# Performance work log

Hardware: AMD Instinct MI355X
Metric: run time of the kernel (lower is better)

Reference implementation:

```python
import jax, jax.numpy as jnp
import numpy as np
from jax import lax

B, C, H, W = 4, 64, 64, 64
CH = C // 2  # edge_detect hidden channels
BN_EPS = 1e-5


def conv1x1(x, w, b):
    # x: (B,C,H,W), w: (O,C), b: (O,)
    return jnp.einsum('bchw,oc->bohw', x, w) + b[None, :, None, None]


def setup_inputs() -> dict:
    key = jax.random.key(0)
    ks = jax.random.split(key, 12)
    s = 1.0 / np.sqrt(C)
    inp = {
        'x': jax.random.normal(ks[0], (B, C, H, W), jnp.float32),
        'Wq': jax.random.normal(ks[1], (C, C), jnp.float32) * s,
        'bq': jnp.zeros((C,), jnp.float32),
        'Wk': jax.random.normal(ks[2], (C, C), jnp.float32) * s,
        'bk': jnp.zeros((C,), jnp.float32),
        'Wv': jax.random.normal(ks[3], (C, C), jnp.float32) * s,
        'bv': jnp.zeros((C,), jnp.float32),
        'We1': jax.random.normal(ks[4], (CH, C, 3, 3), jnp.float32) * (1.0 / np.sqrt(C * 9)),
        'be1': jnp.zeros((CH,), jnp.float32),
        'bn_w': jnp.ones((CH,), jnp.float32),
        'bn_b': jnp.zeros((CH,), jnp.float32),
        'bn_mean': jnp.zeros((CH,), jnp.float32),
        'bn_var': jnp.ones((CH,), jnp.float32),
        'We2': jax.random.normal(ks[5], (1, CH), jnp.float32) * (1.0 / np.sqrt(CH)),
        'be2': jnp.zeros((1,), jnp.float32),
        'gamma': jax.random.normal(ks[6], (1,), jnp.float32) * 0.1,
        'beta': jax.random.normal(ks[7], (1,), jnp.float32) * 0.1,
    }
    return inp


def reference(x, Wq, bq, Wk, bk, Wv, bv, We1, be1, bn_w, bn_b, bn_mean, bn_var, We2, be2, gamma, beta):
    b, c, h, w = x.shape
    hw = h * w
    q = conv1x1(x, Wq, bq).reshape(b, c, hw).transpose(0, 2, 1)  # (B,HW,C)
    k = conv1x1(x, Wk, bk).reshape(b, c, hw)                      # (B,C,HW)
    v = conv1x1(x, Wv, bv).reshape(b, c, hw)                      # (B,C,HW)

    energy = jnp.einsum('bnc,bcm->bnm', q, k)                      # (B,HW,HW)
    attention = jax.nn.softmax(energy, axis=-1)

    # edge_detect: 3x3 conv -> BN (eval stats) -> ReLU -> 1x1 conv -> sigmoid
    e = lax.conv_general_dilated(x, We1, (1, 1), 'SAME',
                                 dimension_numbers=('NCHW', 'OIHW', 'NCHW'))
    e = e + be1[None, :, None, None]
    e = (e - bn_mean[None, :, None, None]) * jax.lax.rsqrt(bn_var + BN_EPS)[None, :, None, None]
    e = e * bn_w[None, :, None, None] + bn_b[None, :, None, None]
    e = jax.nn.relu(e)
    e = conv1x1(e, We2, be2)                                       # (B,1,H,W)
    edge = jax.nn.sigmoid(e).reshape(b, 1, hw)                     # (B,1,HW)

    fa = attention * (1.0 + beta[0] * edge)                        # broadcast over query dim
    denom = jnp.maximum(jnp.sum(jnp.abs(fa), axis=2, keepdims=True), 1e-12)
    fa = fa / denom                                                # L1 renorm along keys

    out = jnp.einsum('bcm,bnm->bcn', v, fa).reshape(b, c, h, w)
    return gamma[0] * out + x
```

## Files before the change

kernel.cpp:

```cpp
#include <hip/hip_runtime.h>
#include <hip/hip_bf16.h>

typedef unsigned short u16;
typedef __attribute__((ext_vector_type(8))) __bf16 bf16x8;
typedef __attribute__((ext_vector_type(4))) float f32x4;


__device__ __forceinline__ u16 f2bf(float f) {
    unsigned u = __builtin_bit_cast(unsigned, f);
    u += 0x7FFFu + ((u >> 16) & 1u);
    return (u16)(u >> 16);
}
__device__ __forceinline__ float bf2f(u16 v) {
    unsigned u = ((unsigned)v) << 16;
    return __builtin_bit_cast(float, u);
}

__global__ __launch_bounds__(256) void qkv_edge_kernel(
    const float* __restrict__ x,
    const float* __restrict__ Wq, const float* __restrict__ bq,
    const float* __restrict__ Wk, const float* __restrict__ bk,
    const float* __restrict__ Wv, const float* __restrict__ bv,
    const float* __restrict__ We1, const float* __restrict__ be1,
    const float* __restrict__ bn_w, const float* __restrict__ bn_b,
    const float* __restrict__ bn_mean, const float* __restrict__ bn_var,
    const float* __restrict__ We2, const float* __restrict__ be2,
    const float* __restrict__ beta,
    u16* __restrict__ Qt, u16* __restrict__ Kt, u16* __restrict__ Vm,
    float* __restrict__ wkey)
{
    __shared__ __align__(16) u16 sm[33280];
    const int t = threadIdx.x;
    const int wv = t >> 6, lane = t & 63;
    const int quad = lane >> 4, l15 = lane & 15;

    if (blockIdx.x < 256) {
        u16* Wl   = sm;
        u16* xt_s = sm + 13824;
        u16* vt   = sm + 13824 + 4224;
        const int b = blockIdx.x >> 6;
        const int n0 = (blockIdx.x & 63) << 6;

        const float* Wmat[3] = {Wq, Wk, Wv};
#pragma unroll
        for (int m = 0; m < 3; ++m)
#pragma unroll
            for (int i = 0; i < 4; ++i) {
                int u = t + i * 256;
                float4 w4 = *reinterpret_cast<const float4*>(Wmat[m] + u * 4);
                int row = u >> 4, col = (u & 15) * 4;
                uint2 pk;
                pk.x = (unsigned)f2bf(w4.x) | ((unsigned)f2bf(w4.y) << 16);
                pk.y = (unsigned)f2bf(w4.z) | ((unsigned)f2bf(w4.w) << 16);
                *reinterpret_cast<uint2*>(&Wl[(m * 64 + row) * 72 + col]) = pk;
            }
        for (int i = 0; i < 16; ++i) {
            int lin = t + i * 256;
            int c = lin >> 6, nn = lin & 63;
            xt_s[nn * 66 + c] = f2bf(x[(size_t)(b * 64 + c) * 4096 + n0 + nn]);
        }
        __syncthreads();

        bf16x8 bx[2];
#pragma unroll
        for (int h = 0; h < 2; ++h)
            bx[h] = *reinterpret_cast<const bf16x8*>(
                &xt_s[(wv * 16 + l15) * 66 + h * 32 + quad * 8]);

        f32x4 d[3][4];
#pragma unroll
        for (int m = 0; m < 3; ++m)
#pragma unroll
            for (int mt = 0; mt < 4; ++mt) d[m][mt] = (f32x4){0.f, 0.f, 0.f, 0.f};

#pragma unroll
        for (int h = 0; h < 2; ++h)
#pragma unroll
            for (int m = 0; m < 3; ++m)
#pragma unroll
                for (int mt = 0; mt < 4; ++mt) {
                    bf16x8 af = *reinterpret_cast<const bf16x8*>(
                        &Wl[(m * 64 + mt * 16 + l15) * 72 + h * 32 + quad * 8]);
                    d[m][mt] = __builtin_amdgcn_mfma_f32_16x16x32_bf16(af, bx[h], d[m][mt], 0, 0, 0);
                }

        const float* bias[3] = {bq, bk, bv};
        const float L2E = 1.44269504f;
#pragma unroll
        for (int m = 0; m < 3; ++m)
#pragma unroll
            for (int mt = 0; mt < 4; ++mt) {
                float4 bi = *reinterpret_cast<const float4*>(bias[m] + mt * 16 + quad * 4);
                d[m][mt][0] += bi.x; d[m][mt][1] += bi.y; d[m][mt][2] += bi.z; d[m][mt][3] += bi.w;
                if (m == 0) {
                    d[m][mt][0] *= L2E; d[m][mt][1] *= L2E;
                    d[m][mt][2] *= L2E; d[m][mt][3] *= L2E;
                }
            }

        const int rowchunk = (n0 >> 4) + wv;
#pragma unroll
        for (int m = 0; m < 2; ++m) {
            u16* base = (m == 0 ? Qt : Kt) + (size_t)b * 262144;
#pragma unroll
            for (int mt = 0; mt < 4; ++mt) {
                uint2 pk;
                pk.x = (unsigned)f2bf(d[m][mt][0]) | ((unsigned)f2bf(d[m][mt][1]) << 16);
                pk.y = (unsigned)f2bf(d[m][mt][2]) | ((unsigned)f2bf(d[m][mt][3]) << 16);
                *reinterpret_cast<uint2*>(
                    base + ((size_t)(rowchunk * 8 + mt * 2 + (quad >> 1))) * 128 +
                    l15 * 8 + (quad & 1) * 4) = pk;
            }
        }
#pragma unroll
        for (int mt = 0; mt < 4; ++mt)
#pragma unroll
            for (int r = 0; r < 4; ++r)
                vt[(mt * 16 + quad * 4 + r) * 72 + wv * 16 + l15] = f2bf(d[2][mt][r]);
        __syncthreads();
        {
            u16* Vb_st = Vm + (size_t)b * 262144;
            const int kt = n0 >> 6;
#pragma unroll
            for (int i = 0; i < 2; ++i) {
                int unit = t + i * 256;
                int f = unit >> 7, hq = (unit >> 4) & 7, cl = unit & 15;
                const u16* src = &vt[(f * 16 + cl) * 72 + hq * 8];
                uint4 v4 = *reinterpret_cast<const uint4*>(src);
                *reinterpret_cast<uint4*>(
                    Vb_st + ((size_t)((kt * 4 + f) * 8 + hq)) * 128 + cl * 8) = v4;
            }
        }
    } else {
        u16* Ae_s = sm;
        u16* xr_s = sm + 18688;
        const int eb = blockIdx.x - 256;
        const int b = eb >> 6, h = eb & 63;

        if (t < 192) {
            int kh = t / 64, rem = t & 63;
            int col = (rem >> 5) * 65, ci2 = (rem & 31) * 2;
            *reinterpret_cast<unsigned*>(&xr_s[(kh * 66 + col) * 72 + ci2]) = 0u;
        }
#pragma unroll
        for (int i = 0; i < 18; ++i) {
            int u = t + i * 256;
            int ch = u / 144;
            int rem = u - ch * 144;
            int p = rem >> 4, cig = (rem & 15) * 4;
            const float* src = We1 + ch * 576 + cig * 9 + p;
            float a = src[0], b2 = src[9], c2 = src[18], d2 = src[27];
            uint2 pk;
            pk.x = (unsigned)f2bf(a) | ((unsigned)f2bf(b2) << 16);
            pk.y = (unsigned)f2bf(c2) | ((unsigned)f2bf(d2) << 16);
            *reinterpret_cast<uint2*>(&Ae_s[ch * 584 + p * 64 + cig]) = pk;
        }
#pragma unroll
        for (int i = 0; i < 12; ++i) {
            int u = t + i * 256;
            int w = u & 63, cig = (u >> 6) & 15, kh = u >> 10;
            int hs = h + kh - 1;
            float v0 = 0.f, v1 = 0.f, v2 = 0.f, v3 = 0.f;
            if ((unsigned)hs < 64u) {
                const float* src = x + ((size_t)(b * 64 + cig * 4) * 64 + hs) * 64 + w;
                v0 = src[0]; v1 = src[4096]; v2 = src[8192]; v3 = src[12288];
            }
            uint2 pk;
            pk.x = (unsigned)f2bf(v0) | ((unsigned)f2bf(v1) << 16);
            pk.y = (unsigned)f2bf(v2) | ((unsigned)f2bf(v3) << 16);
            *reinterpret_cast<uint2*>(&xr_s[(kh * 66 + w + 1) * 72 + cig * 4]) = pk;
        }
        __syncthreads();

        f32x4 e[2];
        e[0] = (f32x4){0.f, 0.f, 0.f, 0.f};
        e[1] = (f32x4){0.f, 0.f, 0.f, 0.f};
#pragma unroll
        for (int p = 0; p < 9; ++p) {
            const int kh = p / 3, kw = p - kh * 3;
#pragma unroll
            for (int half = 0; half < 2; ++half) {
                bf16x8 bfr = *reinterpret_cast<const bf16x8*>(
                    &xr_s[(kh * 66 + wv * 16 + l15 + kw) * 72 + half * 32 + quad * 8]);
#pragma unroll
                for (int mt = 0; mt < 2; ++mt) {
                    bf16x8 af = *reinterpret_cast<const bf16x8*>(
                        &Ae_s[(mt * 16 + l15) * 584 + p * 64 + half * 32 + quad * 8]);
                    e[mt] = __builtin_amdgcn_mfma_f32_16x16x32_bf16(af, bfr, e[mt], 0, 0, 0);
                }
            }
        }
        float partial = 0.f;
#pragma unroll
        for (int mt = 0; mt < 2; ++mt) {
            float4 bw = *reinterpret_cast<const float4*>(bn_w    + mt * 16 + quad * 4);
            float4 bb = *reinterpret_cast<const float4*>(bn_b    + mt * 16 + quad * 4);
            float4 bm = *reinterpret_cast<const float4*>(bn_mean + mt * 16 + quad * 4);
            float4 bv2 = *reinterpret_cast<const float4*>(bn_var + mt * 16 + quad * 4);
            float4 b1 = *reinterpret_cast<const float4*>(be1     + mt * 16 + quad * 4);
            float4 w2 = *reinterpret_cast<const float4*>(We2     + mt * 16 + quad * 4);
            float sc, sh;
            sc = bw.x * rsqrtf(bv2.x + 1e-5f); sh = (b1.x - bm.x) * sc + bb.x;
            partial += fmaxf(e[mt][0] * sc + sh, 0.f) * w2.x;
            sc = bw.y * rsqrtf(bv2.y + 1e-5f); sh = (b1.y - bm.y) * sc + bb.y;
            partial += fmaxf(e[mt][1] * sc + sh, 0.f) * w2.y;
            sc = bw.z * rsqrtf(bv2.z + 1e-5f); sh = (b1.z - bm.z) * sc + bb.z;
            partial += fmaxf(e[mt][2] * sc + sh, 0.f) * w2.z;
            sc = bw.w * rsqrtf(bv2.w + 1e-5f); sh = (b1.w - bm.w) * sc + bb.w;
            partial += fmaxf(e[mt][3] * sc + sh, 0.f) * w2.w;
        }
        partial += __shfl_xor(partial, 16);
        partial += __shfl_xor(partial, 32);
        if (lane < 16) {
            float s = partial + be2[0];
            float sg = 1.f / (1.f + __expf(-s));
            wkey[(size_t)b * 4096 + h * 64 + wv * 16 + lane] = 1.f + beta[0] * sg;
        }
    }
}

template <int NSPLIT>
__global__ __launch_bounds__(128, 4) void attn_kernel(
    const u16* __restrict__ Qt, const u16* __restrict__ Kt,
    const u16* __restrict__ Vm, const float* __restrict__ wkey,
    u16* __restrict__ O_part, float* __restrict__ l_part)
{
    constexpr int KT_ITERS = 64 / NSPLIT;
    __shared__ __align__(16) u16 p_s_all[2 * 32 * 68];
    const int t = threadIdx.x;
    const int qi = blockIdx.x / NSPLIT;
    const int split = blockIdx.x % NSPLIT;
    const int b = qi >> 6;
    const int n0 = (qi & 63) << 6;
    const int wv = t >> 6, lane = t & 63;
    const int quad = lane >> 4, l15 = lane & 15;
    u16* p_s = p_s_all + wv * (32 * 68);

    const u16* Qb = Qt + (size_t)b * 262144;
    const u16* Kb = Kt + (size_t)b * 262144;
    const u16* Vb = Vm + (size_t)b * 262144;
    const float* wb = wkey + (size_t)b * 4096;

    bf16x8 qf[2][2];
#pragma unroll
    for (int nt = 0; nt < 2; ++nt)
#pragma unroll
        for (int h = 0; h < 2; ++h)
            qf[nt][h] = __builtin_bit_cast(bf16x8, *reinterpret_cast<const uint4*>(
                Qb + ((size_t)(((n0 >> 4) + wv * 2 + nt) * 8 + h * 4 + quad)) * 128 + l15 * 8));

    const int kt0 = split * KT_ITERS;
    uint4 kf[4][2];
    float4 wf[4];
#pragma unroll
    for (int mt = 0; mt < 4; ++mt) {
#pragma unroll
        for (int h = 0; h < 2; ++h)
            kf[mt][h] = *reinterpret_cast<const uint4*>(
                Kb + ((size_t)((kt0 * 4 + mt) * 8 + h * 4 + quad)) * 128 + l15 * 8);
        wf[mt] = *reinterpret_cast<const float4*>(wb + kt0 * 64 + mt * 16 + quad * 4);
    }

    f32x4 o[2][4];
#pragma unroll
    for (int m2 = 0; m2 < 2; ++m2)
#pragma unroll
        for (int f = 0; f < 4; ++f) o[m2][f] = (f32x4){0.f, 0.f, 0.f, 0.f};
    float l_acc[2] = {0.f, 0.f};

    for (int kt = kt0; kt < kt0 + KT_ITERS; ++kt) {
        uint4 vf[4][2];
#pragma unroll
        for (int f = 0; f < 4; ++f)
#pragma unroll
            for (int h = 0; h < 2; ++h)
                vf[f][h] = *reinterpret_cast<const uint4*>(
                    Vb + ((size_t)((kt * 4 + f) * 8 + h * 4 + quad)) * 128 + l15 * 8);

        f32x4 s[4][2];
#pragma unroll
        for (int mt = 0; mt < 4; ++mt)
#pragma unroll
            for (int nt = 0; nt < 2; ++nt) {
                f32x4 a = (f32x4){0.f, 0.f, 0.f, 0.f};
                a = __builtin_amdgcn_mfma_f32_16x16x32_bf16(
                        __builtin_bit_cast(bf16x8, kf[mt][0]), qf[nt][0], a, 0, 0, 0);
                a = __builtin_amdgcn_mfma_f32_16x16x32_bf16(
                        __builtin_bit_cast(bf16x8, kf[mt][1]), qf[nt][1], a, 0, 0, 0);
                s[mt][nt] = a;
            }

        const int ktn = (kt + 1 < kt0 + KT_ITERS) ? kt + 1 : kt0;
#pragma unroll
        for (int mt = 0; mt < 4; ++mt)
#pragma unroll
            for (int h = 0; h < 2; ++h)
                kf[mt][h] = *reinterpret_cast<const uint4*>(
                    Kb + ((size_t)((ktn * 4 + mt) * 8 + h * 4 + quad)) * 128 + l15 * 8);

        const float OFF = 17.3123405f;
#pragma unroll
        for (int mt = 0; mt < 4; ++mt) {
            const float* wfp = reinterpret_cast<const float*>(&wf[mt]);
#pragma unroll
            for (int nt = 0; nt < 2; ++nt) {
                float p0 = exp2f(s[mt][nt][0] - OFF) * wfp[0];
                float p1 = exp2f(s[mt][nt][1] - OFF) * wfp[1];
                float p2 = exp2f(s[mt][nt][2] - OFF) * wfp[2];
                float p3 = exp2f(s[mt][nt][3] - OFF) * wfp[3];
                l_acc[nt] += (p0 + p1) + (p2 + p3);
                unsigned u0 = __builtin_bit_cast(unsigned, p0);
                unsigned u1 = __builtin_bit_cast(unsigned, p1);
                unsigned u2 = __builtin_bit_cast(unsigned, p2);
                unsigned u3 = __builtin_bit_cast(unsigned, p3);
                uint2 packed;
                packed.x = (u0 >> 16) | (u1 & 0xFFFF0000u);
                packed.y = (u2 >> 16) | (u3 & 0xFFFF0000u);
                *reinterpret_cast<uint2*>(
                    &p_s[(nt * 16 + l15) * 68 + mt * 16 + quad * 4]) = packed;
            }
        }

#pragma unroll
        for (int mt = 0; mt < 4; ++mt)
            wf[mt] = *reinterpret_cast<const float4*>(wb + ktn * 64 + mt * 16 + quad * 4);

        bf16x8 pa[2][2];
#pragma unroll
        for (int m2 = 0; m2 < 2; ++m2)
#pragma unroll
            for (int h = 0; h < 2; ++h) {
                uint2 lo = *reinterpret_cast<const uint2*>(
                    &p_s[(m2 * 16 + l15) * 68 + h * 32 + quad * 8]);
                uint2 hi = *reinterpret_cast<const uint2*>(
                    &p_s[(m2 * 16 + l15) * 68 + h * 32 + quad * 8 + 4]);
                uint4 c4; c4.x = lo.x; c4.y = lo.y; c4.z = hi.x; c4.w = hi.y;
                pa[m2][h] = __builtin_bit_cast(bf16x8, c4);
            }

#pragma unroll
        for (int m2 = 0; m2 < 2; ++m2)
#pragma unroll
            for (int f = 0; f < 4; ++f) {
                o[m2][f] = __builtin_amdgcn_mfma_f32_16x16x32_bf16(
                    pa[m2][0], __builtin_bit_cast(bf16x8, vf[f][0]), o[m2][f], 0, 0, 0);
                o[m2][f] = __builtin_amdgcn_mfma_f32_16x16x32_bf16(
                    pa[m2][1], __builtin_bit_cast(bf16x8, vf[f][1]), o[m2][f], 0, 0, 0);
            }
    }

    const size_t pbase = (size_t)blockIdx.x * 64;
#pragma unroll
    for (int nt = 0; nt < 2; ++nt) {
        float v = l_acc[nt];
        v += __shfl_xor(v, 16);
        v += __shfl_xor(v, 32);
        if (lane < 16) l_part[pbase + wv * 32 + nt * 16 + lane] = v;
    }
#pragma unroll
    for (int m2 = 0; m2 < 2; ++m2)
#pragma unroll
        for (int f = 0; f < 4; ++f)
#pragma unroll
            for (int r = 0; r < 4; ++r)
                O_part[(pbase + wv * 32 + m2 * 16 + quad * 4 + r) * 64 + f * 16 + l15] =
                    f2bf(o[m2][f][r]);
}

template <int NSPLIT>
__global__ __launch_bounds__(256) void combine_kernel(
    const u16* __restrict__ O_part, const float* __restrict__ l_part,
    const float* __restrict__ x, const float* __restrict__ g_gamma,
    float* __restrict__ out)
{
    __shared__ float ot[16 * 65];
    __shared__ float ls[16];
    const int t = threadIdx.x;
    const int b = blockIdx.x >> 8;
    const int R0 = (blockIdx.x & 255) << 4;
    const int qi = (b << 6) + (R0 >> 6);
    const int ro = R0 & 63;
    const float gamma = g_gamma[0];

    {
        const int r = t >> 4, cq = (t & 15) * 4;
        float a0 = 0.f, a1 = 0.f, a2 = 0.f, a3 = 0.f;
#pragma unroll
        for (int s4 = 0; s4 < NSPLIT; ++s4) {
            const u16* p = O_part +
                (((size_t)qi * NSPLIT + s4) * 64 + ro + r) * 64 + cq;
            uint2 u = *reinterpret_cast<const uint2*>(p);
            a0 += bf2f((u16)(u.x & 0xFFFF));
            a1 += bf2f((u16)(u.x >> 16));
            a2 += bf2f((u16)(u.y & 0xFFFF));
            a3 += bf2f((u16)(u.y >> 16));
        }
        ot[r * 65 + cq + 0] = a0;
        ot[r * 65 + cq + 1] = a1;
        ot[r * 65 + cq + 2] = a2;
        ot[r * 65 + cq + 3] = a3;
        if (t < 16) {
            float lsum = 0.f;
#pragma unroll
            for (int s4 = 0; s4 < NSPLIT; ++s4)
                lsum += l_part[((size_t)qi * NSPLIT + s4) * 64 + ro + t];
            ls[t] = gamma / fmaxf(lsum, 1e-30f);
        }
    }
    __syncthreads();
    {
        const int c = t >> 2, nseg = t & 3;
        const size_t gbase = ((size_t)(b * 64 + c)) * 4096 + R0 + nseg * 4;
        float4 xv = *reinterpret_cast<const float4*>(&x[gbase]);
        float4 rv;
        rv.x = ot[(nseg * 4 + 0) * 65 + c] * ls[nseg * 4 + 0] + xv.x;
        rv.y = ot[(nseg * 4 + 1) * 65 + c] * ls[nseg * 4 + 1] + xv.y;
        rv.z = ot[(nseg * 4 + 2) * 65 + c] * ls[nseg * 4 + 2] + xv.z;
        rv.w = ot[(nseg * 4 + 3) * 65 + c] * ls[nseg * 4 + 3] + xv.w;
        *reinterpret_cast<float4*>(&out[gbase]) = rv;
    }
}

extern "C" void kernel_launch(void* const* d_in, const int* in_sizes, int n_in,
                              void* d_out, int out_size, void* d_ws, size_t ws_size,
                              hipStream_t stream) {
    const float* x      = (const float*)d_in[0];
    const float* Wq     = (const float*)d_in[1];
    const float* bq     = (const float*)d_in[2];
    const float* Wk     = (const float*)d_in[3];
    const float* bk     = (const float*)d_in[4];
    const float* Wv     = (const float*)d_in[5];
    const float* bv     = (const float*)d_in[6];
    const float* We1    = (const float*)d_in[7];
    const float* be1    = (const float*)d_in[8];
    const float* bn_w   = (const float*)d_in[9];
    const float* bn_b   = (const float*)d_in[10];
    const float* bn_mean= (const float*)d_in[11];
    const float* bn_var = (const float*)d_in[12];
    const float* We2    = (const float*)d_in[13];
    const float* be2    = (const float*)d_in[14];
    const float* gamma  = (const float*)d_in[15];
    const float* beta   = (const float*)d_in[16];

    char* ws = (char*)d_ws;
    const size_t KB = 1024, MB = 1024 * 1024;
    u16*   Qt     = (u16*)ws;
    u16*   Kt     = (u16*)(ws + 2 * MB);
    u16*   Vm     = (u16*)(ws + 4 * MB);
    float* wkey   = (float*)(ws + 6 * MB);
    float* l_part = (float*)(ws + 6 * MB + 64 * KB);
    u16*   O_part = (u16*)(ws + 6 * MB + 576 * KB);

    const bool use8 = ws_size >= (6 * MB + 576 * KB + (size_t)2048 * 64 * 64 * 2);

    float* out = (float*)d_out;

    qkv_edge_kernel<<<dim3(512), dim3(256), 0, stream>>>(
        x, Wq, bq, Wk, bk, Wv, bv, We1, be1, bn_w, bn_b, bn_mean, bn_var,
        We2, be2, beta, Qt, Kt, Vm, wkey);
    if (use8) {
        attn_kernel<8><<<dim3(2048), dim3(128), 0, stream>>>(Qt, Kt, Vm, wkey, O_part, l_part);
        combine_kernel<8><<<dim3(1024), dim3(256), 0, stream>>>(O_part, l_part, x, gamma, out);
    } else {
        attn_kernel<4><<<dim3(1024), dim3(128), 0, stream>>>(Qt, Kt, Vm, wkey, O_part, l_part);
        combine_kernel<4><<<dim3(1024), dim3(256), 0, stream>>>(O_part, l_part, x, gamma, out);
    }
}
```

Measured before the change: 155.4 us.

## Compute row sums via MFMA with ones and store partials in fragment-native layout

Replaces the scalar per-lane accumulation of softmax row sums with an extra MFMA against a ones vector, so the sums come from the same bf16-rounded probabilities that feed P@V. The partial output tile is now written in the MFMA fragment order as packed 8-byte stores instead of scattered 2-byte stores. The combine kernel is rewritten to read that layout, with one block per query tile (256 blocks handling 64 rows each). This adds MFMA work to the inner loop and gives the combine step fewer, larger blocks.

```diff
diff --git a/kernel.cpp b/kernel.cpp
--- a/kernel.cpp
+++ b/kernel.cpp
@@ -261,12 +261,17 @@
         wf[mt] = *reinterpret_cast<const float4*>(wb + kt0 * 64 + mt * 16 + quad * 4);
     }
 
+    const uint4 ones_u = {0x3F803F80u, 0x3F803F80u, 0x3F803F80u, 0x3F803F80u};
+    const bf16x8 onesf = __builtin_bit_cast(bf16x8, ones_u);
+
     f32x4 o[2][4];
-#pragma unroll
-    for (int m2 = 0; m2 < 2; ++m2)
+    f32x4 l5[2];
+#pragma unroll
+    for (int m2 = 0; m2 < 2; ++m2) {
 #pragma unroll
         for (int f = 0; f < 4; ++f) o[m2][f] = (f32x4){0.f, 0.f, 0.f, 0.f};
-    float l_acc[2] = {0.f, 0.f};
+        l5[m2] = (f32x4){0.f, 0.f, 0.f, 0.f};
+    }
 
     for (int kt = kt0; kt < kt0 + KT_ITERS; ++kt) {
         uint4 vf[4][2];
@@ -308,7 +313,6 @@
                 float p1 = exp2f(s[mt][nt][1] - OFF) * wfp[1];
                 float p2 = exp2f(s[mt][nt][2] - OFF) * wfp[2];
                 float p3 = exp2f(s[mt][nt][3] - OFF) * wfp[3];
-                l_acc[nt] += (p0 + p1) + (p2 + p3);
                 unsigned u0 = __builtin_bit_cast(unsigned, p0);
                 unsigned u1 = __builtin_bit_cast(unsigned, p1);
                 unsigned u2 = __builtin_bit_cast(unsigned, p2);
@@ -339,7 +343,7 @@
             }
 
 #pragma unroll
-        for (int m2 = 0; m2 < 2; ++m2)
+        for (int m2 = 0; m2 < 2; ++m2) {
 #pragma unroll
             for (int f = 0; f < 4; ++f) {
                 o[m2][f] = __builtin_amdgcn_mfma_f32_16x16x32_bf16(
@@ -347,24 +351,29 @@
                 o[m2][f] = __builtin_amdgcn_mfma_f32_16x16x32_bf16(
                     pa[m2][1], __builtin_bit_cast(bf16x8, vf[f][1]), o[m2][f], 0, 0, 0);
             }
-    }
-
-    const size_t pbase = (size_t)blockIdx.x * 64;
-#pragma unroll
-    for (int nt = 0; nt < 2; ++nt) {
-        float v = l_acc[nt];
-        v += __shfl_xor(v, 16);
-        v += __shfl_xor(v, 32);
-        if (lane < 16) l_part[pbase + wv * 32 + nt * 16 + lane] = v;
-    }
-#pragma unroll
-    for (int m2 = 0; m2 < 2; ++m2)
-#pragma unroll
-        for (int f = 0; f < 4; ++f)
-#pragma unroll
-            for (int r = 0; r < 4; ++r)
-                O_part[(pbase + wv * 32 + m2 * 16 + quad * 4 + r) * 64 + f * 16 + l15] =
-                    f2bf(o[m2][f][r]);
+            l5[m2] = __builtin_amdgcn_mfma_f32_16x16x32_bf16(pa[m2][0], onesf, l5[m2], 0, 0, 0);
+            l5[m2] = __builtin_amdgcn_mfma_f32_16x16x32_bf16(pa[m2][1], onesf, l5[m2], 0, 0, 0);
+        }
+    }
+
+    const size_t pbase = (size_t)blockIdx.x * 4096;
+#pragma unroll
+    for (int m2 = 0; m2 < 2; ++m2) {
+        if (l15 == 0) {
+            float4 lv;
+            lv.x = l5[m2][0]; lv.y = l5[m2][1]; lv.z = l5[m2][2]; lv.w = l5[m2][3];
+            *reinterpret_cast<float4*>(
+                &l_part[(size_t)blockIdx.x * 64 + wv * 32 + m2 * 16 + quad * 4]) = lv;
+        }
+#pragma unroll
+        for (int f = 0; f < 4; ++f) {
+            uint2 pk;
+            pk.x = (unsigned)f2bf(o[m2][f][0]) | ((unsigned)f2bf(o[m2][f][1]) << 16);
+            pk.y = (unsigned)f2bf(o[m2][f][2]) | ((unsigned)f2bf(o[m2][f][3]) << 16);
+            *reinterpret_cast<uint2*>(
+                &O_part[pbase + ((((wv * 2 + m2) * 4 + f) * 4 + quad)) * 64 + l15 * 4]) = pk;
+        }
+    }
 }
 
 template <int NSPLIT>
@@ -373,51 +382,67 @@
     const float* __restrict__ x, const float* __restrict__ g_gamma,
     float* __restrict__ out)
 {
-    __shared__ float ot[16 * 65];
-    __shared__ float ls[16];
+    __shared__ float ot[64 * 65];
+    __shared__ float ls[64];
     const int t = threadIdx.x;
-    const int b = blockIdx.x >> 8;
-    const int R0 = (blockIdx.x & 255) << 4;
-    const int qi = (b << 6) + (R0 >> 6);
-    const int ro = R0 & 63;
+    const int qi = blockIdx.x;
+    const int b = qi >> 6;
+    const int n0 = (qi & 63) << 6;
+    const int f = t >> 6, quad = (t >> 4) & 3, l15 = t & 15;
     const float gamma = g_gamma[0];
 
-    {
-        const int r = t >> 4, cq = (t & 15) * 4;
-        float a0 = 0.f, a1 = 0.f, a2 = 0.f, a3 = 0.f;
-#pragma unroll
-        for (int s4 = 0; s4 < NSPLIT; ++s4) {
-            const u16* p = O_part +
-                (((size_t)qi * NSPLIT + s4) * 64 + ro + r) * 64 + cq;
-            uint2 u = *reinterpret_cast<const uint2*>(p);
-            a0 += bf2f((u16)(u.x & 0xFFFF));
-            a1 += bf2f((u16)(u.x >> 16));
-            a2 += bf2f((u16)(u.y & 0xFFFF));
-            a3 += bf2f((u16)(u.y >> 16));
-        }
-        ot[r * 65 + cq + 0] = a0;
-        ot[r * 65 + cq + 1] = a1;
-        ot[r * 65 + cq + 2] = a2;
-        ot[r * 65 + cq + 3] = a3;
-        if (t < 16) {
-            float lsum = 0.f;
-#pragma unroll
-            for (int s4 = 0; s4 < NSPLIT; ++s4)
-                lsum += l_part[((size_t)qi * NSPLIT + s4) * 64 + ro + t];
-            ls[t] = gamma / fmaxf(lsum, 1e-30f);
-        }
+    float acc[2][2][4];
+#pragma unroll
+    for (int wv = 0; wv < 2; ++wv)
+#pragma unroll
+        for (int m2 = 0; m2 < 2; ++m2)
+#pragma unroll
+            for (int r = 0; r < 4; ++r) acc[wv][m2][r] = 0.f;
+
+#pragma unroll
+    for (int s4 = 0; s4 < NSPLIT; ++s4) {
+        const u16* base = O_part + ((size_t)(qi * NSPLIT + s4)) * 4096;
+#pragma unroll
+        for (int wv = 0; wv < 2; ++wv)
+#pragma unroll
+            for (int m2 = 0; m2 < 2; ++m2) {
+                uint2 u = *reinterpret_cast<const uint2*>(
+                    base + ((((wv * 2 + m2) * 4 + f) * 4 + quad)) * 64 + l15 * 4);
+                acc[wv][m2][0] += bf2f((u16)(u.x & 0xFFFF));
+                acc[wv][m2][1] += bf2f((u16)(u.x >> 16));
+                acc[wv][m2][2] += bf2f((u16)(u.y & 0xFFFF));
+                acc[wv][m2][3] += bf2f((u16)(u.y >> 16));
+            }
+    }
+#pragma unroll
+    for (int wv = 0; wv < 2; ++wv)
+#pragma unroll
+        for (int m2 = 0; m2 < 2; ++m2)
+#pragma unroll
+            for (int r = 0; r < 4; ++r)
+                ot[(wv * 32 + m2 * 16 + quad * 4 + r) * 65 + f * 16 + l15] = acc[wv][m2][r];
+    if (t < 64) {
+        float lsum = 0.f;
+#pragma unroll
+        for (int s4 = 0; s4 < NSPLIT; ++s4)
+            lsum += l_part[((size_t)(qi * NSPLIT + s4)) * 64 + t];
+        ls[t] = gamma / fmaxf(lsum, 1e-30f);
     }
     __syncthreads();
     {
         const int c = t >> 2, nseg = t & 3;
-        const size_t gbase = ((size_t)(b * 64 + c)) * 4096 + R0 + nseg * 4;
-        float4 xv = *reinterpret_cast<const float4*>(&x[gbase]);
-        float4 rv;
-        rv.x = ot[(nseg * 4 + 0) * 65 + c] * ls[nseg * 4 + 0] + xv.x;
-        rv.y = ot[(nseg * 4 + 1) * 65 + c] * ls[nseg * 4 + 1] + xv.y;
-        rv.z = ot[(nseg * 4 + 2) * 65 + c] * ls[nseg * 4 + 2] + xv.z;
-        rv.w = ot[(nseg * 4 + 3) * 65 + c] * ls[nseg * 4 + 3] + xv.w;
-        *reinterpret_cast<float4*>(&out[gbase]) = rv;
+        const size_t gbase = ((size_t)(b * 64 + c)) * 4096 + n0 + nseg * 16;
+#pragma unroll
+        for (int j = 0; j < 4; ++j) {
+            float4 xv = *reinterpret_cast<const float4*>(&x[gbase + j * 4]);
+            float4 rv;
+            int nl = nseg * 16 + j * 4;
+            rv.x = ot[(nl + 0) * 65 + c] * ls[nl + 0] + xv.x;
+            rv.y = ot[(nl + 1) * 65 + c] * ls[nl + 1] + xv.y;
+            rv.z = ot[(nl + 2) * 65 + c] * ls[nl + 2] + xv.z;
+            rv.w = ot[(nl + 3) * 65 + c] * ls[nl + 3] + xv.w;
+            *reinterpret_cast<float4*>(&out[gbase + j * 4]) = rv;
+        }
     }
 }
 
@@ -460,9 +485,9 @@
         We2, be2, beta, Qt, Kt, Vm, wkey);
     if (use8) {
         attn_kernel<8><<<dim3(2048), dim3(128), 0, stream>>>(Qt, Kt, Vm, wkey, O_part, l_part);
-        combine_kernel<8><<<dim3(1024), dim3(256), 0, stream>>>(O_part, l_part, x, gamma, out);
+        combine_kernel<8><<<dim3(256), dim3(256), 0, stream>>>(O_part, l_part, x, gamma, out);
     } else {
         attn_kernel<4><<<dim3(1024), dim3(128), 0, stream>>>(Qt, Kt, Vm, wkey, O_part, l_part);
-        combine_kernel<4><<<dim3(1024), dim3(256), 0, stream>>>(O_part, l_part, x, gamma, out);
-    }
-}
+        combine_kernel<4><<<dim3(256), dim3(256), 0, stream>>>(O_part, l_part, x, gamma, out);
+    }
+}
```

New measurement: 148.6 us. -4.4%, faster.
